# Performance work log

Measured on AMD Instinct MI355X. Metric: run time of the kernel, lower is better.

## Reference

```python
import jax, jax.numpy as jnp
import numpy as np

B, L, D, T = 2, 2048, 1536, 2
INITRANGE = 0.1

def setup_inputs() -> dict:
    key = jax.random.key(0)
    k1, k2 = jax.random.split(key)
    hidden_states = jax.random.normal(k1, (B, L, D), dtype=jnp.float32)
    # decoder: Linear(2*D, T) with uniform(-0.1, 0.1) weight, zero bias
    W = jax.random.uniform(k2, (T, 2 * D), dtype=jnp.float32, minval=-INITRANGE, maxval=INITRANGE)
    b = jnp.zeros((T,), dtype=jnp.float32)
    return {"hidden_states": hidden_states, "W": W, "b": b}

def reference(hidden_states, W, b):
    # Faithful fused version of:
    #   prod = h[:,:,None,:] * h[:,None,:,:]; diff = h[:,:,None,:] - h[:,None,:,:]
    #   logits = cat(prod, diff, -1) @ W.T + b
    # Split W into the product half and the difference half.
    d = hidden_states.shape[-1]
    Wp, Wd = W[:, :d], W[:, d:]                      # [T, D] each
    # prod term: sum_d h[b,i,d] * h[b,j,d] * Wp[t,d]
    hw = jnp.einsum('bid,td->btid', hidden_states, Wp)          # [B,T,L,D]
    prod_logits = jnp.einsum('btid,bjd->bijt', hw, hidden_states)  # [B,L,L,T]
    # diff term: (h[b,i]-h[b,j]) @ Wd.T = (h@Wd.T)[b,i] - (h@Wd.T)[b,j]
    hd = jnp.einsum('bid,td->bit', hidden_states, Wd)           # [B,L,T]
    diff_logits = hd[:, :, None, :] - hd[:, None, :, :]         # [B,L,L,T]
    logits = prod_logits + diff_logits + b
    # symmetrize over the (i, j) pair axes
    logits = (logits + jnp.transpose(logits, (0, 2, 1, 3))) * 0.5
    return logits
```

## Files before the change

kernel.cpp:

```cpp
#include <hip/hip_runtime.h>
#include <hip/hip_bf16.h>
#include <stdint.h>

#define B_ 2
#define L_ 2048
#define D_ 1536

typedef __attribute__((ext_vector_type(4))) float  f32x4;
typedef __attribute__((ext_vector_type(8))) __bf16 bf16x8;

__device__ __forceinline__ unsigned short f2bf(float f) {
  unsigned int u = __float_as_uint(f);
  u += 0x7fffu + ((u >> 16) & 1u);
  return (unsigned short)(u >> 16);
}

__global__ __launch_bounds__(256) void conv_kernel(
    const float* __restrict__ hs, const float* __restrict__ W,
    unsigned short* __restrict__ X, unsigned short* __restrict__ P) {
  const int idx  = blockIdx.x * 256 + threadIdx.x;
  const int base = idx * 4;
  const int d    = base % D_;
  const float4 h  = *(const float4*)(hs + base);
  const float4 w0 = *(const float4*)(W + d);
  const float4 w1 = *(const float4*)(W + 2 * D_ + d);
  ushort4 x, p0, p1;
  x.x  = f2bf(h.x);        x.y  = f2bf(h.y);        x.z  = f2bf(h.z);        x.w  = f2bf(h.w);
  p0.x = f2bf(h.x * w0.x); p0.y = f2bf(h.y * w0.y); p0.z = f2bf(h.z * w0.z); p0.w = f2bf(h.w * w0.w);
  p1.x = f2bf(h.x * w1.x); p1.y = f2bf(h.y * w1.y); p1.z = f2bf(h.z * w1.z); p1.w = f2bf(h.w * w1.w);
  *(ushort4*)(X + base) = x;
  *(ushort4*)(P + base) = p0;
  *(ushort4*)(P + (size_t)B_ * L_ * D_ + base) = p1;
}

__device__ __forceinline__ void gload16(const unsigned short* g, unsigned short* l) {
  __builtin_amdgcn_global_load_lds(
      (const __attribute__((address_space(1))) unsigned int*)g,
      (__attribute__((address_space(3))) unsigned int*)l, 16, 0, 0);
}

#define B0O 0
#define B1O 16384
#define B2O 32768
#define B3O 49152

__global__ __launch_bounds__(512, 2) void gemm_kernel(
    const unsigned short* __restrict__ X, const unsigned short* __restrict__ P,
    const float* __restrict__ bias, float2* __restrict__ out) {
  __shared__ unsigned short lds[65536];

  const int tid = threadIdx.x;

  const int id  = blockIdx.x;
  const int swz = (id & 7) * 32 + (id >> 3);
  const int bz  = swz >> 7;
  const int t2  = swz & 127;
  const int I0  = (t2 >> 3) * 128;
  const int J0  = (t2 & 7) * 256;

  const size_t planeB = (size_t)B_ * L_ * D_;

  const size_t gsrcOff = (size_t)(tid >> 2) * D_ +
                         (size_t)((((tid & 3) ^ ((tid >> 3) & 3))) * 8);
  const unsigned short* sA0 = P + (size_t)(bz * L_ + I0) * D_ + gsrcOff;
  const unsigned short* sA1 = sA0 + planeB;
  const unsigned short* sB0 = X + (size_t)(bz * L_ + J0) * D_ + gsrcOff;
  const unsigned short* sB1 = sB0 + (size_t)128 * D_;
  const int wuni = (tid >> 6) * 512;

  const int lane = tid & 63;
  const int w    = tid >> 6;
  const int wr   = w & 1;
  const int wc   = w >> 1;
  const int lr   = lane & 15;
  const int q    = lane >> 4;
  const int slot8 = ((q ^ ((lr >> 1) & 3)) * 8);
  int aOff[8], bOff[4];
#pragma unroll
  for (int m = 0; m < 8; ++m)
    aOff[m] = (m >> 2) * 4096 + (wr * 64 + (m & 3) * 16 + lr) * 32;
#pragma unroll
  for (int n = 0; n < 4; ++n)
    bOff[n] = 8192 + (n >> 1) * 4096 + (wc * 32 + (n & 1) * 16 + lr) * 32;

  f32x4  acc[8][4] = {};
  bf16x8 aF[8], bF[4];

#define STG4(NB, PN)                                                          \
  do {                                                                        \
    const size_t ko = (size_t)((PN) * 32);                                    \
    gload16(sA0 + ko, lds + (NB) + 0     + wuni);                             \
    gload16(sA1 + ko, lds + (NB) + 4096  + wuni);                             \
    gload16(sB0 + ko, lds + (NB) + 8192  + wuni);                             \
    gload16(sB1 + ko, lds + (NB) + 12288 + wuni);                             \
  } while (0)

#define RDALL(CB)                                                             \
  do {                                                                        \
    const unsigned short* base_ = lds + (CB) + slot8;                         \
    _Pragma("unroll") for (int m = 0; m < 8; ++m)                             \
      aF[m] = *(const bf16x8*)(base_ + aOff[m]);                              \
    _Pragma("unroll") for (int n = 0; n < 4; ++n)                             \
      bF[n] = *(const bf16x8*)(base_ + bOff[n]);                              \
  } while (0)

#define MMALL()                                                               \
  do {                                                                        \
    _Pragma("unroll") for (int m = 0; m < 8; ++m)                             \
      _Pragma("unroll") for (int n = 0; n < 4; ++n)                           \
        acc[m][n] = __builtin_amdgcn_mfma_f32_16x16x32_bf16(                  \
            aF[m], bF[n], acc[m][n], 0, 0, 0);                                \
  } while (0)

#define BNDRY()                                                               \
  do {                                                                        \
    asm volatile("s_waitcnt vmcnt(0)" ::: "memory");                          \
    __builtin_amdgcn_s_barrier();                                             \
    __builtin_amdgcn_sched_barrier(0);                                        \
  } while (0)

#define PRIO1() __builtin_amdgcn_s_setprio(1)
#define PRIO0() __builtin_amdgcn_s_setprio(0)

#define PHR(CB)                                                               \
  do {                                                                        \
    RDALL(CB);                                                                \
    PRIO1(); MMALL(); PRIO0();                                                \
  } while (0)

  STG4(B0O, 0);
  STG4(B1O, 1);

#pragma unroll 1
  for (int it = 0; it < 11; ++it) {
    const int p0 = 4 * it;
    BNDRY();
    STG4(B2O, p0 + 2); STG4(B3O, p0 + 3);
    PHR(B0O); PHR(B1O);
    BNDRY();
    STG4(B0O, p0 + 4); STG4(B1O, p0 + 5);
    PHR(B2O); PHR(B3O);
  }

  BNDRY();
  STG4(B2O, 46); STG4(B3O, 47);
  PHR(B0O); PHR(B1O);
  BNDRY();
  PHR(B2O); PHR(B3O);

#undef PHR
#undef BNDRY
#undef STG4
#undef RDALL
#undef MMALL

  const float bias0 = bias[0], bias1 = bias[1];
#pragma unroll
  for (int m = 0; m < 4; ++m) {
#pragma unroll
    for (int r = 0; r < 4; ++r) {
      const int i = I0 + wr * 64 + m * 16 + q * 4 + r;
      float2* orow = out + (size_t)(bz * L_ + i) * L_;
#pragma unroll
      for (int n = 0; n < 4; ++n) {
        const int j = J0 + (n >> 1) * 128 + wc * 32 + (n & 1) * 16 + lr;
        float2 v;
        v.x = acc[m][n][r] + bias0;
        v.y = acc[m + 4][n][r] + bias1;
        orow[j] = v;
      }
    }
  }
}

extern "C" void kernel_launch(void* const* d_in, const int* in_sizes, int n_in,
                              void* d_out, int out_size, void* d_ws, size_t ws_size,
                              hipStream_t stream) {
  const float* hs   = (const float*)d_in[0];
  const float* W    = (const float*)d_in[1];
  const float* bias = (const float*)d_in[2];

  unsigned short* X = (unsigned short*)d_ws;
  unsigned short* P = X + (size_t)B_ * L_ * D_;

  const int nconv = (B_ * L_ * D_ / 4) / 256;
  conv_kernel<<<nconv, 256, 0, stream>>>(hs, W, X, P);

  gemm_kernel<<<256, 512, 0, stream>>>(X, P, bias, (float2*)d_out);
}
```

Before: 139.9 us.

## Shrink GEMM tiles to 64x128 with 256-thread blocks and triple-buffered LDS pipeline

The GEMM moves from 256 blocks of 512 threads, each computing a 128x256 output tile for both planes, to 1024 blocks of 256 threads computing 64x128 tiles. LDS drops to 48 KB so up to three blocks can share a CU. The K loop changes from a double-pair buffer with two barriers per four phases to a three-stage ring. Each phase reads fragments, issues the next global-to-LDS load, runs MFMAs, then does a partial vmcnt wait and a single barrier. The aim is more occupancy, better latency hiding and finer load balance across CUs, at the cost of less operand reuse per block and more total global/L2 traffic.

New measurement: 150.4 us. +7.6%, slower.

```diff
diff --git a/kernel.cpp b/kernel.cpp
--- a/kernel.cpp
+++ b/kernel.cpp
@@ -40,33 +40,31 @@
 }
 
 #define B0O 0
-#define B1O 16384
-#define B2O 32768
-#define B3O 49152
+#define B1O 8192
+#define B2O 16384
 
-__global__ __launch_bounds__(512, 2) void gemm_kernel(
+__global__ __launch_bounds__(256, 3) void gemm_kernel(
     const unsigned short* __restrict__ X, const unsigned short* __restrict__ P,
     const float* __restrict__ bias, float2* __restrict__ out) {
-  __shared__ unsigned short lds[65536];
+  __shared__ unsigned short lds[24576];
 
   const int tid = threadIdx.x;
 
   const int id  = blockIdx.x;
-  const int swz = (id & 7) * 32 + (id >> 3);
-  const int bz  = swz >> 7;
-  const int t2  = swz & 127;
-  const int I0  = (t2 >> 3) * 128;
-  const int J0  = (t2 & 7) * 256;
+  const int swz = (id & 7) * 128 + (id >> 3);
+  const int bz  = swz >> 9;
+  const int t2  = swz & 511;
+  const int I0  = (t2 >> 4) * 64;
+  const int J0  = (t2 & 15) * 128;
 
   const size_t planeB = (size_t)B_ * L_ * D_;
 
-  const size_t gsrcOff = (size_t)(tid >> 2) * D_ +
-                         (size_t)((((tid & 3) ^ ((tid >> 3) & 3))) * 8);
-  const unsigned short* sA0 = P + (size_t)(bz * L_ + I0) * D_ + gsrcOff;
-  const unsigned short* sA1 = sA0 + planeB;
-  const unsigned short* sB0 = X + (size_t)(bz * L_ + J0) * D_ + gsrcOff;
-  const unsigned short* sB1 = sB0 + (size_t)128 * D_;
-  const int wuni = (tid >> 6) * 512;
+  const int    csrc = (((tid & 3) ^ ((tid >> 3) & 3))) * 8;
+  const unsigned short* pA0 = P + (size_t)(tid >> 7) * planeB +
+                              (size_t)(bz * L_ + I0 + ((tid >> 2) & 31)) * D_ + csrc;
+  const unsigned short* pA1 = pA0 + (size_t)32 * D_;
+  const unsigned short* pB0 = X + (size_t)(bz * L_ + J0 + (tid >> 2)) * D_ + csrc;
+  const unsigned short* pB1 = pB0 + (size_t)64 * D_;
 
   const int lane = tid & 63;
   const int w    = tid >> 6;
@@ -74,31 +72,29 @@
   const int wc   = w >> 1;
   const int lr   = lane & 15;
   const int q    = lane >> 4;
-  const int slot8 = ((q ^ ((lr >> 1) & 3)) * 8);
-  int aOff[8], bOff[4];
+  const int slot8 = (q ^ ((lr >> 1) & 3)) * 8;
+  int aOff[4], bOff[4];
 #pragma unroll
-  for (int m = 0; m < 8; ++m)
-    aOff[m] = (m >> 2) * 4096 + (wr * 64 + (m & 3) * 16 + lr) * 32;
+  for (int m = 0; m < 4; ++m) aOff[m] = (wr * 64 + m * 16 + lr) * 32;
 #pragma unroll
-  for (int n = 0; n < 4; ++n)
-    bOff[n] = 8192 + (n >> 1) * 4096 + (wc * 32 + (n & 1) * 16 + lr) * 32;
+  for (int n = 0; n < 4; ++n) bOff[n] = 4096 + (wc * 64 + n * 16 + lr) * 32;
 
-  f32x4  acc[8][4] = {};
-  bf16x8 aF[8], bF[4];
+  f32x4  acc[4][4] = {};
+  bf16x8 aF[4], bF[4];
 
-#define STG4(NB, PN)                                                          \
+#define STG(NB, PN)                                                           \
   do {                                                                        \
     const size_t ko = (size_t)((PN) * 32);                                    \
-    gload16(sA0 + ko, lds + (NB) + 0     + wuni);                             \
-    gload16(sA1 + ko, lds + (NB) + 4096  + wuni);                             \
-    gload16(sB0 + ko, lds + (NB) + 8192  + wuni);                             \
-    gload16(sB1 + ko, lds + (NB) + 12288 + wuni);                             \
+    gload16(pA0 + ko, lds + (NB) + tid * 8);                                  \
+    gload16(pA1 + ko, lds + (NB) + 2048 + tid * 8);                           \
+    gload16(pB0 + ko, lds + (NB) + 4096 + tid * 8);                           \
+    gload16(pB1 + ko, lds + (NB) + 6144 + tid * 8);                           \
   } while (0)
 
 #define RDALL(CB)                                                             \
   do {                                                                        \
     const unsigned short* base_ = lds + (CB) + slot8;                         \
-    _Pragma("unroll") for (int m = 0; m < 8; ++m)                             \
+    _Pragma("unroll") for (int m = 0; m < 4; ++m)                             \
       aF[m] = *(const bf16x8*)(base_ + aOff[m]);                              \
     _Pragma("unroll") for (int n = 0; n < 4; ++n)                             \
       bF[n] = *(const bf16x8*)(base_ + bOff[n]);                              \
@@ -106,68 +102,68 @@
 
 #define MMALL()                                                               \
   do {                                                                        \
-    _Pragma("unroll") for (int m = 0; m < 8; ++m)                             \
+    _Pragma("unroll") for (int m = 0; m < 4; ++m)                             \
       _Pragma("unroll") for (int n = 0; n < 4; ++n)                           \
         acc[m][n] = __builtin_amdgcn_mfma_f32_16x16x32_bf16(                  \
             aF[m], bF[n], acc[m][n], 0, 0, 0);                                \
   } while (0)
 
-#define BNDRY()                                                               \
+#define WVM(n)  asm volatile("s_waitcnt vmcnt(" #n ")" ::: "memory")
+#define BARS()                                                                \
   do {                                                                        \
-    asm volatile("s_waitcnt vmcnt(0)" ::: "memory");                          \
     __builtin_amdgcn_s_barrier();                                             \
     __builtin_amdgcn_sched_barrier(0);                                        \
   } while (0)
-
 #define PRIO1() __builtin_amdgcn_s_setprio(1)
 #define PRIO0() __builtin_amdgcn_s_setprio(0)
 
-#define PHR(CB)                                                               \
+#define PH(CB, SB, PN)                                                        \
   do {                                                                        \
     RDALL(CB);                                                                \
+    STG(SB, PN);                                                              \
     PRIO1(); MMALL(); PRIO0();                                                \
+    WVM(4); BARS();                                                           \
   } while (0)
 
-  STG4(B0O, 0);
-  STG4(B1O, 1);
+  STG(B0O, 0);
+  STG(B1O, 1);
+  WVM(4);
+  BARS();
 
 #pragma unroll 1
-  for (int it = 0; it < 11; ++it) {
-    const int p0 = 4 * it;
-    BNDRY();
-    STG4(B2O, p0 + 2); STG4(B3O, p0 + 3);
-    PHR(B0O); PHR(B1O);
-    BNDRY();
-    STG4(B0O, p0 + 4); STG4(B1O, p0 + 5);
-    PHR(B2O); PHR(B3O);
+  for (int it = 0; it < 15; ++it) {
+    const int p0 = 3 * it;
+    PH(B0O, B2O, p0 + 2);
+    PH(B1O, B0O, p0 + 3);
+    PH(B2O, B1O, p0 + 4);
   }
+  RDALL(B0O); STG(B2O, 47);
+  PRIO1(); MMALL(); PRIO0();
+  WVM(4); BARS();
+  RDALL(B1O);
+  PRIO1(); MMALL(); PRIO0();
+  WVM(0); BARS();
+  RDALL(B2O);
+  PRIO1(); MMALL(); PRIO0();
 
-  BNDRY();
-  STG4(B2O, 46); STG4(B3O, 47);
-  PHR(B0O); PHR(B1O);
-  BNDRY();
-  PHR(B2O); PHR(B3O);
-
-#undef PHR
-#undef BNDRY
-#undef STG4
+#undef PH
+#undef STG
 #undef RDALL
 #undef MMALL
 
   const float bias0 = bias[0], bias1 = bias[1];
 #pragma unroll
-  for (int m = 0; m < 4; ++m) {
+  for (int m = 0; m < 2; ++m) {
 #pragma unroll
     for (int r = 0; r < 4; ++r) {
-      const int i = I0 + wr * 64 + m * 16 + q * 4 + r;
-      float2* orow = out + (size_t)(bz * L_ + i) * L_;
+      const int i = I0 + wr * 32 + m * 16 + q * 4 + r;
+      float2* orow = out + (size_t)(bz * L_ + i) * L_ + (J0 + wc * 64 + lr);
 #pragma unroll
       for (int n = 0; n < 4; ++n) {
-        const int j = J0 + (n >> 1) * 128 + wc * 32 + (n & 1) * 16 + lr;
         float2 v;
         v.x = acc[m][n][r] + bias0;
-        v.y = acc[m + 4][n][r] + bias1;
-        orow[j] = v;
+        v.y = acc[m + 2][n][r] + bias1;
+        orow[n * 16] = v;
       }
     }
   }
@@ -186,5 +182,5 @@
   const int nconv = (B_ * L_ * D_ / 4) / 256;
   conv_kernel<<<nconv, 256, 0, stream>>>(hs, W, X, P);
 
-  gemm_kernel<<<256, 512, 0, stream>>>(X, P, bias, (float2*)d_out);
+  gemm_kernel<<<1024, 256, 0, stream>>>(X, P, bias, (float2*)d_out);
 }
```
